# Optimization experiments

Hardware: AMD Instinct MI355X
Metric: run time of the kernel (lower is better)

The kernel has to match this reference:

```python
import jax, jax.numpy as jnp
import numpy as np

EPS = 1e-5
SLOPE = 0.2


def _conv_bn_lrelu(x, w, b, g, be, m, v):
    # 1x1 conv: (B,C,H,W) x (O,C) -> (B,O,H,W), then BN (inference) + LeakyReLU(0.2)
    y = jnp.einsum('bchw,oc->bohw', x, w) + b[None, :, None, None]
    y = g[None, :, None, None] * (y - m[None, :, None, None]) * jax.lax.rsqrt(v[None, :, None, None] + EPS) + be[None, :, None, None]
    return jnp.where(y >= 0, y, SLOPE * y)


def setup_inputs() -> dict:
    key = jax.random.key(0)
    ks = jax.random.split(key, 20)
    B, C, H, W = 8, 64, 256, 256
    d = {}
    d['x'] = jax.random.normal(ks[0], (B, C, H, W), dtype=jnp.float32)
    d['w1'] = jax.random.normal(ks[1], (1, C), dtype=jnp.float32) * 0.1
    d['b1'] = jax.random.normal(ks[2], (1,), dtype=jnp.float32)
    d['g1'] = jax.random.uniform(ks[3], (1,), dtype=jnp.float32) + 0.5
    d['be1'] = jax.random.normal(ks[4], (1,), dtype=jnp.float32)
    d['m1'] = jax.random.normal(ks[5], (1,), dtype=jnp.float32)
    d['v1'] = jax.random.uniform(ks[6], (1,), dtype=jnp.float32) + 0.5
    d['wA'] = jax.random.normal(ks[7], (C, C), dtype=jnp.float32) * 0.1
    d['bA'] = jax.random.normal(ks[8], (C,), dtype=jnp.float32)
    d['gA'] = jax.random.uniform(ks[9], (C,), dtype=jnp.float32) + 0.5
    d['beA'] = jax.random.normal(ks[10], (C,), dtype=jnp.float32)
    d['mA'] = jax.random.normal(ks[11], (C,), dtype=jnp.float32)
    d['vA'] = jax.random.uniform(ks[12], (C,), dtype=jnp.float32) + 0.5
    d['wO'] = jax.random.normal(ks[13], (C, C), dtype=jnp.float32) * 0.1
    d['bO'] = jax.random.normal(ks[14], (C,), dtype=jnp.float32)
    d['gO'] = jax.random.uniform(ks[15], (C,), dtype=jnp.float32) + 0.5
    d['beO'] = jax.random.normal(ks[16], (C,), dtype=jnp.float32)
    d['mO'] = jax.random.normal(ks[17], (C,), dtype=jnp.float32)
    d['vO'] = jax.random.uniform(ks[18], (C,), dtype=jnp.float32) + 0.5
    return d


def reference(x, w1, b1, g1, be1, m1, v1, wA, bA, gA, beA, mA, vA, wO, bO, gO, beO, mO, vO):
    B, C, H, W = x.shape
    # Branch 1: C->1 conv + BN + LeakyReLU, squeeze channel -> (B,H,W)
    C1 = _conv_bn_lrelu(x, w1, b1, g1, be1, m1, v1)[:, 0]  # (B,H,W)
    C1_t = jnp.swapaxes(C1, 1, 2)                           # (B,W,H)
    S1 = jax.nn.softmax(jnp.matmul(C1, C1_t), axis=-1)      # (B,H,H)
    S2 = jax.nn.softmax(jnp.matmul(C1_t, C1), axis=-1)      # (B,W,W)
    # Branch 2: C->C conv + BN + LeakyReLU
    C2 = _conv_bn_lrelu(x, wA, bA, gA, beA, mA, vA)         # (B,C,H,W)
    # Raw row-major reshapes as in the torch code (mixes channel and spatial dims)
    R1 = C2.reshape(B, H, C * W)
    R2 = C2.reshape(B, W, C * H)
    R3 = jnp.matmul(S1, R1).reshape(B, C, H, W)
    R4 = jnp.matmul(S2, R2).reshape(B, C, H, W)
    C3 = _conv_bn_lrelu(R3 + R4, wO, bO, gO, beO, mO, vO)
    out = C2 + C3
    return (out, S1, S2)
```

## Files before the change

### kernel.cpp

```cpp
#include <hip/hip_runtime.h>


#define EPS 1e-5f

typedef __attribute__((ext_vector_type(8))) short bf16x8;
typedef __attribute__((ext_vector_type(4))) float f32x4;

__device__ __forceinline__ unsigned short f2bf(float f){
  union { float f; unsigned int u; } a; a.f = f;
  return (unsigned short)((a.u + 0x7fffu + ((a.u >> 16) & 1u)) >> 16);
}
__device__ __forceinline__ float bf2f(unsigned short u){
  union { unsigned int i; float f; } v; v.i = ((unsigned int)u) << 16; return v.f;
}
__device__ __forceinline__ float lrelu(float y){ return y >= 0.f ? y : 0.2f * y; }
__device__ __forceinline__ bf16x8 cvt8(const float* p){
  float4 a = *(const float4*)p;
  float4 b = *(const float4*)(p + 4);
  bf16x8 r;
  r[0] = (short)f2bf(a.x); r[1] = (short)f2bf(a.y); r[2] = (short)f2bf(a.z); r[3] = (short)f2bf(a.w);
  r[4] = (short)f2bf(b.x); r[5] = (short)f2bf(b.y); r[6] = (short)f2bf(b.z); r[7] = (short)f2bf(b.w);
  return r;
}

__global__ __launch_bounds__(256, 2) void k1_front(
    const float* __restrict__ x,
    const float* __restrict__ w1,
    const float* __restrict__ pb1, const float* __restrict__ pg1,
    const float* __restrict__ pbe1, const float* __restrict__ pm1,
    const float* __restrict__ pv1,
    const float* __restrict__ wA, const float* __restrict__ pbA,
    const float* __restrict__ pgA, const float* __restrict__ pbeA,
    const float* __restrict__ pmA, const float* __restrict__ pvA,
    float* __restrict__ C2out, float* __restrict__ C1)
{
  const int blk = blockIdx.x;
  const int b  = blk >> 8;
  const int n0 = (blk & 255) << 8;
  const int t  = threadIdx.x;
  const int lane = t & 63;
  const int wv = t >> 6;
  const int m = lane & 15;
  const int q = lane >> 4;

  __shared__ float w1s[64];
  __shared__ float sAl[64], tAl[64];
  if (t < 64){
    w1s[t] = w1[t];
    float s = pgA[t] * rsqrtf(pvA[t] + EPS);
    sAl[t] = s;
    tAl[t] = (pbA[t] - pmA[t]) * s + pbeA[t];
  }
  __syncthreads();

  float sAv[4], tAv[4];
  #pragma unroll
  for (int ot = 0; ot < 4; ot++){ sAv[ot] = sAl[16*ot + m]; tAv[ot] = tAl[16*ot + m]; }

  bf16x8 wfr[4][2];
  #pragma unroll
  for (int ot = 0; ot < 4; ot++)
    #pragma unroll
    for (int ks = 0; ks < 2; ks++)
      wfr[ot][ks] = cvt8(wA + (16*ot + m)*64 + ks*32 + q*8);

  const f32x4 vzero = {0.f, 0.f, 0.f, 0.f};
  f32x4 acc[4][4];
  #pragma unroll
  for (int i = 0; i < 4; i++)
    #pragma unroll
    for (int j = 0; j < 4; j++) acc[i][j] = vzero;

  const float* xb = x + ((size_t)b << 22);
  const int nbase = n0 + 64*wv;

  #pragma unroll
  for (int ks = 0; ks < 2; ks++){
    #pragma unroll
    for (int nt = 0; nt < 4; nt++){
      const int n = nbase + 16*nt + m;
      bf16x8 af;
      #pragma unroll
      for (int u = 0; u < 8; u++){
        const int c = ks*32 + q*8 + u;
        af[u] = (short)f2bf(xb[((size_t)c << 16) + n]);
      }
      #pragma unroll
      for (int ot = 0; ot < 4; ot++)
        acc[nt][ot] = __builtin_amdgcn_mfma_f32_16x16x32_bf16(af, wfr[ot][ks], acc[nt][ot], 0, 0, 0);
    }
  }

  const size_t outB = ((size_t)b << 22);
  #pragma unroll
  for (int nt = 0; nt < 4; nt++)
    #pragma unroll
    for (int ot = 0; ot < 4; ot++){
      float4 pk;
      pk.x = lrelu(acc[nt][ot][0] * sAv[ot] + tAv[ot]);
      pk.y = lrelu(acc[nt][ot][1] * sAv[ot] + tAv[ot]);
      pk.z = lrelu(acc[nt][ot][2] * sAv[ot] + tAv[ot]);
      pk.w = lrelu(acc[nt][ot][3] * sAv[ot] + tAv[ot]);
      *(float4*)(C2out + outB + ((size_t)(16*ot + m) << 16) + nbase + 16*nt + 4*q) = pk;
    }

  const float s1 = pg1[0] * rsqrtf(pv1[0] + EPS);
  const float t1 = (pb1[0] - pm1[0]) * s1 + pbe1[0];
  float d = 0.f;
  #pragma unroll 8
  for (int c = 0; c < 64; c++)
    d += xb[((size_t)c << 16) + n0 + t] * w1s[c];
  C1[(b << 16) + n0 + t] = lrelu(d * s1 + t1);
}

__global__ __launch_bounds__(256) void k2_gram(const float* __restrict__ C1, float* __restrict__ G)
{
  const int bx = blockIdx.x;
  const int b = bx >> 5;
  const int which = (bx >> 4) & 1;
  const int tile = bx & 15;
  const int i0 = (tile >> 2) << 6, j0 = (tile & 3) << 6;
  const float* Cb = C1 + (b << 16);
  __shared__ float Al[32][68];
  __shared__ float Bl[32][68];
  const int t = threadIdx.x;
  const int tx = t & 15, ty = t >> 4;
  float acc[4][4];
  #pragma unroll
  for (int i = 0; i < 4; i++)
    #pragma unroll
    for (int j = 0; j < 4; j++) acc[i][j] = 0.f;

  for (int kc = 0; kc < 8; kc++){
    const int k0 = kc << 5;
    __syncthreads();
    if (which == 0){
      const int i = t & 63, kq = t >> 6;
      const float* pa = Cb + (i0 + i)*256 + k0 + kq*8;
      const float* pb = Cb + (j0 + i)*256 + k0 + kq*8;
      #pragma unroll
      for (int u = 0; u < 8; u++){ Al[kq*8+u][i] = pa[u]; Bl[kq*8+u][i] = pb[u]; }
    } else {
      const int k = t >> 3, i8 = (t & 7) << 3;
      const float* pa = Cb + (k0 + k)*256 + i0 + i8;
      const float* pb = Cb + (k0 + k)*256 + j0 + i8;
      *(float4*)&Al[k][i8]   = *(const float4*)pa;
      *(float4*)&Al[k][i8+4] = *(const float4*)(pa+4);
      *(float4*)&Bl[k][i8]   = *(const float4*)pb;
      *(float4*)&Bl[k][i8+4] = *(const float4*)(pb+4);
    }
    __syncthreads();
    #pragma unroll 4
    for (int k = 0; k < 32; k++){
      float4 a4 = *(const float4*)&Al[k][ty << 2];
      float4 b4 = *(const float4*)&Bl[k][tx << 2];
      float av[4] = {a4.x, a4.y, a4.z, a4.w};
      float bw[4] = {b4.x, b4.y, b4.z, b4.w};
      #pragma unroll
      for (int ii = 0; ii < 4; ii++)
        #pragma unroll
        for (int jj = 0; jj < 4; jj++)
          acc[ii][jj] = fmaf(av[ii], bw[jj], acc[ii][jj]);
    }
  }
  float* Go = G + ((size_t)(which*8 + b) << 16);
  #pragma unroll
  for (int r = 0; r < 4; r++){
    float4 o4 = {acc[r][0], acc[r][1], acc[r][2], acc[r][3]};
    *(float4*)&Go[(i0 + (ty<<2) + r)*256 + j0 + (tx<<2)] = o4;
  }
}

__global__ __launch_bounds__(256) void k2_softmax(const float* __restrict__ G,
    float* __restrict__ S1o, float* __restrict__ S2o,
    unsigned short* __restrict__ Ssum2)
{
  const int bx = blockIdx.x;
  const int b = bx >> 8, i = bx & 255;
  const int j = threadIdx.x;
  const float v1 = G[((size_t)b << 16) + i*256 + j];
  const float v2 = G[((size_t)(8 + b) << 16) + i*256 + j];
  __shared__ float sm[4], sm2[4], ss[4], ss2[4];
  float a1 = v1, a2 = v2;
  #pragma unroll
  for (int off = 32; off > 0; off >>= 1){
    a1 = fmaxf(a1, __shfl_xor(a1, off));
    a2 = fmaxf(a2, __shfl_xor(a2, off));
  }
  const int wv = j >> 6;
  if ((j & 63) == 0){ sm[wv] = a1; sm2[wv] = a2; }
  __syncthreads();
  const float m1v = fmaxf(fmaxf(sm[0], sm[1]), fmaxf(sm[2], sm[3]));
  const float m2v = fmaxf(fmaxf(sm2[0], sm2[1]), fmaxf(sm2[2], sm2[3]));
  float e1 = __expf(v1 - m1v), e2 = __expf(v2 - m2v);
  float s1 = e1, s2 = e2;
  #pragma unroll
  for (int off = 32; off > 0; off >>= 1){
    s1 += __shfl_xor(s1, off);
    s2 += __shfl_xor(s2, off);
  }
  if ((j & 63) == 0){ ss[wv] = s1; ss2[wv] = s2; }
  __syncthreads();
  const float d1 = ss[0]+ss[1]+ss[2]+ss[3];
  const float d2 = ss2[0]+ss2[1]+ss2[2]+ss2[3];
  const float S1v = e1 / d1, S2v = e2 / d2;
  S1o[((size_t)b << 16) + i*256 + j] = S1v;
  S2o[((size_t)b << 16) + i*256 + j] = S2v;
  const int ip = ((i & 3) << 6) | (i >> 2);
  const int kp = ((j & 3) << 6) | (j >> 2);
  Ssum2[((size_t)b << 16) + ip*256 + kp] = f2bf(S1v + S2v);
}

__global__ __launch_bounds__(256, 2) void k3_main(
    const unsigned short* __restrict__ Ssum2,
    const float* __restrict__ wO, const float* __restrict__ pbO,
    const float* __restrict__ pgO, const float* __restrict__ pbeO,
    const float* __restrict__ pmO, const float* __restrict__ pvO,
    float* out)
{
  __shared__ unsigned short C2L[256][72];
  __shared__ unsigned short T_lds[256][72];
  __shared__ float sOl[64], tOl[64];
  const int blk = blockIdx.x;
  const int b  = blk >> 8;
  const int j0 = (blk & 255) << 6;
  const int t = threadIdx.x;
  const int lane = t & 63, wv = t >> 6;
  const int m = lane & 15, q = lane >> 4;

  if (t < 64){
    float s = pgO[t] * rsqrtf(pvO[t] + EPS);
    sOl[t] = s;
    tOl[t] = (pbO[t] - pmO[t]) * s + pbeO[t];
  }

  const size_t outB = ((size_t)b << 22);

  #pragma unroll
  for (int it8 = 0; it8 < 8; it8++){
    const int f = it8*256 + t;
    const int c = f >> 5;
    const int p = f & 31;
    const int rk = p >> 3, ch = p & 7;
    const float* src = out + outB + ((size_t)c << 16) + (rk << 14) + j0 + ch*8;
    const float4 v0 = *(const float4*)src;
    const float4 v1 = *(const float4*)(src + 4);
    const int s0 = rk*64 + ch*8;
    C2L[s0+0][c] = f2bf(v0.x); C2L[s0+1][c] = f2bf(v0.y);
    C2L[s0+2][c] = f2bf(v0.z); C2L[s0+3][c] = f2bf(v0.w);
    C2L[s0+4][c] = f2bf(v1.x); C2L[s0+5][c] = f2bf(v1.y);
    C2L[s0+6][c] = f2bf(v1.z); C2L[s0+7][c] = f2bf(v1.w);
  }
  __syncthreads();

  const unsigned short* Sb = Ssum2 + ((size_t)b << 16);

  const f32x4 vzero = {0.f,0.f,0.f,0.f};
  f32x4 acc[4][4];
  #pragma unroll
  for (int i = 0; i < 4; i++)
    #pragma unroll
    for (int j = 0; j < 4; j++) acc[i][j] = vzero;

  #pragma unroll
  for (int ks = 0; ks < 8; ks++){
    const int kk = ks*32 + q*8;
    const int rk = kk >> 6;
    const int c0 = kk & 63;
    bf16x8 af[4], bv[4];
    #pragma unroll
    for (int it = 0; it < 4; it++)
      af[it] = *(const bf16x8*)(Sb + (64*wv + 16*it + m)*256 + kk);
    #pragma unroll
    for (int jt = 0; jt < 4; jt++)
      bv[jt] = *(const bf16x8*)&C2L[(rk << 6) + 16*jt + m][c0];
    #pragma unroll
    for (int it = 0; it < 4; it++)
      #pragma unroll
      for (int jt = 0; jt < 4; jt++)
        acc[it][jt] = __builtin_amdgcn_mfma_f32_16x16x32_bf16(af[it], bv[jt], acc[it][jt], 0, 0, 0);
  }

  #pragma unroll
  for (int it = 0; it < 4; it++)
    #pragma unroll
    for (int jt = 0; jt < 4; jt++){
      uint2 pk;
      pk.x = (unsigned)f2bf(acc[it][jt][0]) | ((unsigned)f2bf(acc[it][jt][1]) << 16);
      pk.y = (unsigned)f2bf(acc[it][jt][2]) | ((unsigned)f2bf(acc[it][jt][3]) << 16);
      *(uint2*)&T_lds[64*wv + 16*jt + m][16*it + 4*q] = pk;
    }
  __syncthreads();

  bf16x8 wfr[4][2];
  #pragma unroll
  for (int ct = 0; ct < 4; ct++)
    #pragma unroll
    for (int k2 = 0; k2 < 2; k2++)
      wfr[ct][k2] = cvt8(wO + (16*ct + m)*64 + k2*32 + q*8);

  f32x4 acc2[4][4];
  #pragma unroll
  for (int i = 0; i < 4; i++)
    #pragma unroll
    for (int j = 0; j < 4; j++) acc2[i][j] = vzero;

  #pragma unroll
  for (int k2 = 0; k2 < 2; k2++)
    #pragma unroll
    for (int stl = 0; stl < 4; stl++){
      const bf16x8 afT = *(const bf16x8*)&T_lds[64*wv + 16*stl + m][k2*32 + q*8];
      #pragma unroll
      for (int ct = 0; ct < 4; ct++)
        acc2[stl][ct] = __builtin_amdgcn_mfma_f32_16x16x32_bf16(afT, wfr[ct][k2], acc2[stl][ct], 0, 0, 0);
    }

  float sOv[4], tOv[4];
  #pragma unroll
  for (int ct = 0; ct < 4; ct++){ sOv[ct] = sOl[16*ct + m]; tOv[ct] = tOl[16*ct + m]; }

  #pragma unroll
  for (int stl = 0; stl < 4; stl++)
    #pragma unroll
    for (int ct = 0; ct < 4; ct++){
      const int cout = 16*ct + m;
      const int ng0 = (wv << 14) + j0 + 16*stl + 4*q;
      float* po = out + outB + ((size_t)cout << 16) + ng0;
      const float4 c2v = *(const float4*)po;
      float4 pk;
      pk.x = c2v.x + lrelu(acc2[stl][ct][0] * sOv[ct] + tOv[ct]);
      pk.y = c2v.y + lrelu(acc2[stl][ct][1] * sOv[ct] + tOv[ct]);
      pk.z = c2v.z + lrelu(acc2[stl][ct][2] * sOv[ct] + tOv[ct]);
      pk.w = c2v.w + lrelu(acc2[stl][ct][3] * sOv[ct] + tOv[ct]);
      *(float4*)po = pk;
    }
}

extern "C" void kernel_launch(void* const* d_in, const int* in_sizes, int n_in,
                              void* d_out, int out_size, void* d_ws, size_t ws_size,
                              hipStream_t stream) {
  const float* x   = (const float*)d_in[0];
  const float* w1  = (const float*)d_in[1];
  const float* b1  = (const float*)d_in[2];
  const float* g1  = (const float*)d_in[3];
  const float* be1 = (const float*)d_in[4];
  const float* m1  = (const float*)d_in[5];
  const float* v1  = (const float*)d_in[6];
  const float* wA  = (const float*)d_in[7];
  const float* bA  = (const float*)d_in[8];
  const float* gA  = (const float*)d_in[9];
  const float* beA = (const float*)d_in[10];
  const float* mA  = (const float*)d_in[11];
  const float* vA  = (const float*)d_in[12];
  const float* wO  = (const float*)d_in[13];
  const float* bO  = (const float*)d_in[14];
  const float* gO  = (const float*)d_in[15];
  const float* beO = (const float*)d_in[16];
  const float* mO  = (const float*)d_in[17];
  const float* vO  = (const float*)d_in[18];

  float* out = (float*)d_out;

  char* ws = (char*)d_ws;
  float* C1             = (float*)(ws);
  float* G              = (float*)(ws + (size_t)(2u << 20));
  unsigned short* Ssum2 = (unsigned short*)(ws + (size_t)(6u << 20));

  k1_front<<<dim3(2048), dim3(256), 0, stream>>>(x, w1, b1, g1, be1, m1, v1,
                                                 wA, bA, gA, beA, mA, vA, out, C1);
  k2_gram<<<dim3(256), dim3(256), 0, stream>>>(C1, G);
  k2_softmax<<<dim3(2048), dim3(256), 0, stream>>>(G, out + 33554432u, out + 34078720u, Ssum2);
  k3_main<<<dim3(2048), dim3(256), 0, stream>>>(Ssum2, wO, bO, gO, beO, mO, vO, out);
}
```

Baseline: 433.7 us.

## Fuse C2 conv into main kernel, recompute from x instead of round-tripping output

The C->C conv+BN+LeakyReLU is moved from the front kernel into k3_main. Each block computes its C2 tile from x with MFMA and keeps it in registers and LDS, instead of writing C2 to global memory and reading it back twice (once for the bf16 staging, once for the residual add). The front kernel shrinks to the C->1 projection using float4 loads. The cost is longer k3 blocks with more register pressure, since c2r accumulators stay live across both GEMMs, plus strided scalar x loads inside k3. One block barrier between the T_lds writes and reads is also dropped.

```diff
diff --git a/kernel.cpp b/kernel.cpp
--- a/kernel.cpp
+++ b/kernel.cpp
@@ -9,9 +9,6 @@
 __device__ __forceinline__ unsigned short f2bf(float f){
   union { float f; unsigned int u; } a; a.f = f;
   return (unsigned short)((a.u + 0x7fffu + ((a.u >> 16) & 1u)) >> 16);
-}
-__device__ __forceinline__ float bf2f(unsigned short u){
-  union { unsigned int i; float f; } v; v.i = ((unsigned int)u) << 16; return v.f;
 }
 __device__ __forceinline__ float lrelu(float y){ return y >= 0.f ? y : 0.2f * y; }
 __device__ __forceinline__ bf16x8 cvt8(const float* p){
@@ -23,94 +20,36 @@
   return r;
 }
 
-__global__ __launch_bounds__(256, 2) void k1_front(
-    const float* __restrict__ x,
-    const float* __restrict__ w1,
+__global__ __launch_bounds__(256) void k1_c1(
+    const float* __restrict__ x, const float* __restrict__ w1,
     const float* __restrict__ pb1, const float* __restrict__ pg1,
     const float* __restrict__ pbe1, const float* __restrict__ pm1,
     const float* __restrict__ pv1,
-    const float* __restrict__ wA, const float* __restrict__ pbA,
-    const float* __restrict__ pgA, const float* __restrict__ pbeA,
-    const float* __restrict__ pmA, const float* __restrict__ pvA,
-    float* __restrict__ C2out, float* __restrict__ C1)
+    float* __restrict__ C1)
 {
   const int blk = blockIdx.x;
-  const int b  = blk >> 8;
-  const int n0 = (blk & 255) << 8;
-  const int t  = threadIdx.x;
-  const int lane = t & 63;
-  const int wv = t >> 6;
-  const int m = lane & 15;
-  const int q = lane >> 4;
-
+  const int b = blk >> 6;
+  const int n0 = (blk & 63) << 10;
+  const int t = threadIdx.x;
   __shared__ float w1s[64];
-  __shared__ float sAl[64], tAl[64];
-  if (t < 64){
-    w1s[t] = w1[t];
-    float s = pgA[t] * rsqrtf(pvA[t] + EPS);
-    sAl[t] = s;
-    tAl[t] = (pbA[t] - pmA[t]) * s + pbeA[t];
-  }
-  __syncthreads();
-
-  float sAv[4], tAv[4];
-  #pragma unroll
-  for (int ot = 0; ot < 4; ot++){ sAv[ot] = sAl[16*ot + m]; tAv[ot] = tAl[16*ot + m]; }
-
-  bf16x8 wfr[4][2];
-  #pragma unroll
-  for (int ot = 0; ot < 4; ot++)
-    #pragma unroll
-    for (int ks = 0; ks < 2; ks++)
-      wfr[ot][ks] = cvt8(wA + (16*ot + m)*64 + ks*32 + q*8);
-
-  const f32x4 vzero = {0.f, 0.f, 0.f, 0.f};
-  f32x4 acc[4][4];
-  #pragma unroll
-  for (int i = 0; i < 4; i++)
-    #pragma unroll
-    for (int j = 0; j < 4; j++) acc[i][j] = vzero;
-
+  if (t < 64) w1s[t] = w1[t];
+  __syncthreads();
   const float* xb = x + ((size_t)b << 22);
-  const int nbase = n0 + 64*wv;
-
-  #pragma unroll
-  for (int ks = 0; ks < 2; ks++){
-    #pragma unroll
-    for (int nt = 0; nt < 4; nt++){
-      const int n = nbase + 16*nt + m;
-      bf16x8 af;
-      #pragma unroll
-      for (int u = 0; u < 8; u++){
-        const int c = ks*32 + q*8 + u;
-        af[u] = (short)f2bf(xb[((size_t)c << 16) + n]);
-      }
-      #pragma unroll
-      for (int ot = 0; ot < 4; ot++)
-        acc[nt][ot] = __builtin_amdgcn_mfma_f32_16x16x32_bf16(af, wfr[ot][ks], acc[nt][ot], 0, 0, 0);
-    }
-  }
-
-  const size_t outB = ((size_t)b << 22);
-  #pragma unroll
-  for (int nt = 0; nt < 4; nt++)
-    #pragma unroll
-    for (int ot = 0; ot < 4; ot++){
-      float4 pk;
-      pk.x = lrelu(acc[nt][ot][0] * sAv[ot] + tAv[ot]);
-      pk.y = lrelu(acc[nt][ot][1] * sAv[ot] + tAv[ot]);
-      pk.z = lrelu(acc[nt][ot][2] * sAv[ot] + tAv[ot]);
-      pk.w = lrelu(acc[nt][ot][3] * sAv[ot] + tAv[ot]);
-      *(float4*)(C2out + outB + ((size_t)(16*ot + m) << 16) + nbase + 16*nt + 4*q) = pk;
-    }
-
+  const int n = n0 + (t << 2);
+  float4 d = {0.f, 0.f, 0.f, 0.f};
+  #pragma unroll 8
+  for (int c = 0; c < 64; c++){
+    const float4 xv = *(const float4*)(xb + ((size_t)c << 16) + n);
+    const float wv = w1s[c];
+    d.x = fmaf(xv.x, wv, d.x); d.y = fmaf(xv.y, wv, d.y);
+    d.z = fmaf(xv.z, wv, d.z); d.w = fmaf(xv.w, wv, d.w);
+  }
   const float s1 = pg1[0] * rsqrtf(pv1[0] + EPS);
   const float t1 = (pb1[0] - pm1[0]) * s1 + pbe1[0];
-  float d = 0.f;
-  #pragma unroll 8
-  for (int c = 0; c < 64; c++)
-    d += xb[((size_t)c << 16) + n0 + t] * w1s[c];
-  C1[(b << 16) + n0 + t] = lrelu(d * s1 + t1);
+  float4 o;
+  o.x = lrelu(d.x * s1 + t1); o.y = lrelu(d.y * s1 + t1);
+  o.z = lrelu(d.z * s1 + t1); o.w = lrelu(d.w * s1 + t1);
+  *(float4*)(C1 + (b << 16) + n) = o;
 }
 
 __global__ __launch_bounds__(256) void k2_gram(const float* __restrict__ C1, float* __restrict__ G)
@@ -212,15 +151,19 @@
 }
 
 __global__ __launch_bounds__(256, 2) void k3_main(
+    const float* __restrict__ x,
+    const float* __restrict__ wA, const float* __restrict__ pbA,
+    const float* __restrict__ pgA, const float* __restrict__ pbeA,
+    const float* __restrict__ pmA, const float* __restrict__ pvA,
     const unsigned short* __restrict__ Ssum2,
     const float* __restrict__ wO, const float* __restrict__ pbO,
     const float* __restrict__ pgO, const float* __restrict__ pbeO,
     const float* __restrict__ pmO, const float* __restrict__ pvO,
-    float* out)
+    float* __restrict__ out)
 {
   __shared__ unsigned short C2L[256][72];
   __shared__ unsigned short T_lds[256][72];
-  __shared__ float sOl[64], tOl[64];
+  __shared__ float sAl[64], tAl[64], sOl[64], tOl[64];
   const int blk = blockIdx.x;
   const int b  = blk >> 8;
   const int j0 = (blk & 255) << 6;
@@ -229,38 +172,66 @@
   const int m = lane & 15, q = lane >> 4;
 
   if (t < 64){
-    float s = pgO[t] * rsqrtf(pvO[t] + EPS);
-    sOl[t] = s;
-    tOl[t] = (pbO[t] - pmO[t]) * s + pbeO[t];
-  }
-
-  const size_t outB = ((size_t)b << 22);
-
-  #pragma unroll
-  for (int it8 = 0; it8 < 8; it8++){
-    const int f = it8*256 + t;
-    const int c = f >> 5;
-    const int p = f & 31;
-    const int rk = p >> 3, ch = p & 7;
-    const float* src = out + outB + ((size_t)c << 16) + (rk << 14) + j0 + ch*8;
-    const float4 v0 = *(const float4*)src;
-    const float4 v1 = *(const float4*)(src + 4);
-    const int s0 = rk*64 + ch*8;
-    C2L[s0+0][c] = f2bf(v0.x); C2L[s0+1][c] = f2bf(v0.y);
-    C2L[s0+2][c] = f2bf(v0.z); C2L[s0+3][c] = f2bf(v0.w);
-    C2L[s0+4][c] = f2bf(v1.x); C2L[s0+5][c] = f2bf(v1.y);
-    C2L[s0+6][c] = f2bf(v1.z); C2L[s0+7][c] = f2bf(v1.w);
-  }
+    const float sA = pgA[t] * rsqrtf(pvA[t] + EPS);
+    sAl[t] = sA; tAl[t] = (pbA[t] - pmA[t]) * sA + pbeA[t];
+    const float sO = pgO[t] * rsqrtf(pvO[t] + EPS);
+    sOl[t] = sO; tOl[t] = (pbO[t] - pmO[t]) * sO + pbeO[t];
+  }
+  __syncthreads();
+
+  float sAv[4], tAv[4];
+  #pragma unroll
+  for (int ot = 0; ot < 4; ot++){ sAv[ot] = sAl[16*ot + m]; tAv[ot] = tAl[16*ot + m]; }
+
+  bf16x8 wfrA[4][2];
+  #pragma unroll
+  for (int ot = 0; ot < 4; ot++)
+    #pragma unroll
+    for (int ks = 0; ks < 2; ks++)
+      wfrA[ot][ks] = cvt8(wA + (16*ot + m)*64 + ks*32 + q*8);
+
+  const f32x4 vzero = {0.f, 0.f, 0.f, 0.f};
+  f32x4 c2r[4][4];
+  #pragma unroll
+  for (int i = 0; i < 4; i++)
+    #pragma unroll
+    for (int j = 0; j < 4; j++) c2r[i][j] = vzero;
+
+  const float* xb = x + ((size_t)b << 22) + (wv << 14) + j0;
+  #pragma unroll
+  for (int ks = 0; ks < 2; ks++)
+    #pragma unroll
+    for (int nt = 0; nt < 4; nt++){
+      bf16x8 af;
+      #pragma unroll
+      for (int u = 0; u < 8; u++){
+        const int cin = ks*32 + q*8 + u;
+        af[u] = (short)f2bf(xb[((size_t)cin << 16) + 16*nt + m]);
+      }
+      #pragma unroll
+      for (int ot = 0; ot < 4; ot++)
+        c2r[nt][ot] = __builtin_amdgcn_mfma_f32_16x16x32_bf16(af, wfrA[ot][ks], c2r[nt][ot], 0, 0, 0);
+    }
+
+  #pragma unroll
+  for (int nt = 0; nt < 4; nt++)
+    #pragma unroll
+    for (int ot = 0; ot < 4; ot++){
+      #pragma unroll
+      for (int r = 0; r < 4; r++){
+        const float v = lrelu(c2r[nt][ot][r] * sAv[ot] + tAv[ot]);
+        c2r[nt][ot][r] = v;
+        C2L[64*wv + 16*nt + 4*q + r][16*ot + m] = f2bf(v);
+      }
+    }
   __syncthreads();
 
   const unsigned short* Sb = Ssum2 + ((size_t)b << 16);
-
-  const f32x4 vzero = {0.f,0.f,0.f,0.f};
-  f32x4 acc[4][4];
+  f32x4 accT[4][4];
   #pragma unroll
   for (int i = 0; i < 4; i++)
     #pragma unroll
-    for (int j = 0; j < 4; j++) acc[i][j] = vzero;
+    for (int j = 0; j < 4; j++) accT[i][j] = vzero;
 
   #pragma unroll
   for (int ks = 0; ks < 8; ks++){
@@ -278,7 +249,7 @@
     for (int it = 0; it < 4; it++)
       #pragma unroll
       for (int jt = 0; jt < 4; jt++)
-        acc[it][jt] = __builtin_amdgcn_mfma_f32_16x16x32_bf16(af[it], bv[jt], acc[it][jt], 0, 0, 0);
+        accT[it][jt] = __builtin_amdgcn_mfma_f32_16x16x32_bf16(af[it], bv[jt], accT[it][jt], 0, 0, 0);
   }
 
   #pragma unroll
@@ -286,18 +257,17 @@
     #pragma unroll
     for (int jt = 0; jt < 4; jt++){
       uint2 pk;
-      pk.x = (unsigned)f2bf(acc[it][jt][0]) | ((unsigned)f2bf(acc[it][jt][1]) << 16);
-      pk.y = (unsigned)f2bf(acc[it][jt][2]) | ((unsigned)f2bf(acc[it][jt][3]) << 16);
+      pk.x = (unsigned)f2bf(accT[it][jt][0]) | ((unsigned)f2bf(accT[it][jt][1]) << 16);
+      pk.y = (unsigned)f2bf(accT[it][jt][2]) | ((unsigned)f2bf(accT[it][jt][3]) << 16);
       *(uint2*)&T_lds[64*wv + 16*jt + m][16*it + 4*q] = pk;
     }
-  __syncthreads();
-
-  bf16x8 wfr[4][2];
+
+  bf16x8 wfrO[4][2];
   #pragma unroll
   for (int ct = 0; ct < 4; ct++)
     #pragma unroll
     for (int k2 = 0; k2 < 2; k2++)
-      wfr[ct][k2] = cvt8(wO + (16*ct + m)*64 + k2*32 + q*8);
+      wfrO[ct][k2] = cvt8(wO + (16*ct + m)*64 + k2*32 + q*8);
 
   f32x4 acc2[4][4];
   #pragma unroll
@@ -312,13 +282,14 @@
       const bf16x8 afT = *(const bf16x8*)&T_lds[64*wv + 16*stl + m][k2*32 + q*8];
       #pragma unroll
       for (int ct = 0; ct < 4; ct++)
-        acc2[stl][ct] = __builtin_amdgcn_mfma_f32_16x16x32_bf16(afT, wfr[ct][k2], acc2[stl][ct], 0, 0, 0);
+        acc2[stl][ct] = __builtin_amdgcn_mfma_f32_16x16x32_bf16(afT, wfrO[ct][k2], acc2[stl][ct], 0, 0, 0);
     }
 
   float sOv[4], tOv[4];
   #pragma unroll
   for (int ct = 0; ct < 4; ct++){ sOv[ct] = sOl[16*ct + m]; tOv[ct] = tOl[16*ct + m]; }
 
+  const size_t outB = ((size_t)b << 22);
   #pragma unroll
   for (int stl = 0; stl < 4; stl++)
     #pragma unroll
@@ -326,12 +297,11 @@
       const int cout = 16*ct + m;
       const int ng0 = (wv << 14) + j0 + 16*stl + 4*q;
       float* po = out + outB + ((size_t)cout << 16) + ng0;
-      const float4 c2v = *(const float4*)po;
       float4 pk;
-      pk.x = c2v.x + lrelu(acc2[stl][ct][0] * sOv[ct] + tOv[ct]);
-      pk.y = c2v.y + lrelu(acc2[stl][ct][1] * sOv[ct] + tOv[ct]);
-      pk.z = c2v.z + lrelu(acc2[stl][ct][2] * sOv[ct] + tOv[ct]);
-      pk.w = c2v.w + lrelu(acc2[stl][ct][3] * sOv[ct] + tOv[ct]);
+      pk.x = c2r[stl][ct][0] + lrelu(acc2[stl][ct][0] * sOv[ct] + tOv[ct]);
+      pk.y = c2r[stl][ct][1] + lrelu(acc2[stl][ct][1] * sOv[ct] + tOv[ct]);
+      pk.z = c2r[stl][ct][2] + lrelu(acc2[stl][ct][2] * sOv[ct] + tOv[ct]);
+      pk.w = c2r[stl][ct][3] + lrelu(acc2[stl][ct][3] * sOv[ct] + tOv[ct]);
       *(float4*)po = pk;
     }
 }
@@ -366,9 +336,9 @@
   float* G              = (float*)(ws + (size_t)(2u << 20));
   unsigned short* Ssum2 = (unsigned short*)(ws + (size_t)(6u << 20));
 
-  k1_front<<<dim3(2048), dim3(256), 0, stream>>>(x, w1, b1, g1, be1, m1, v1,
-                                                 wA, bA, gA, beA, mA, vA, out, C1);
+  k1_c1<<<dim3(512), dim3(256), 0, stream>>>(x, w1, b1, g1, be1, m1, v1, C1);
   k2_gram<<<dim3(256), dim3(256), 0, stream>>>(C1, G);
   k2_softmax<<<dim3(2048), dim3(256), 0, stream>>>(G, out + 33554432u, out + 34078720u, Ssum2);
-  k3_main<<<dim3(2048), dim3(256), 0, stream>>>(Ssum2, wO, bO, gO, beO, mO, vO, out);
-}
+  k3_main<<<dim3(2048), dim3(256), 0, stream>>>(x, wA, bA, gA, beA, mA, vA, Ssum2,
+                                                wO, bO, gO, beO, mO, vO, out);
+}
```

Result: faster. 364.0 us (-16.1%).
